# Optimization experiments

Measured on AMD Instinct MI355X. Metric: run time of the kernel, lower is better.

Reference implementation:

```python
import jax, jax.numpy as jnp
import numpy as np

D = 48


def setup_inputs() -> dict:
    key = jax.random.key(0)
    k1, k2, k3, k4, k5 = jax.random.split(key, 5)
    B, N, d = 4, 512, D
    x = jax.random.normal(k1, (B, N, d), dtype=jnp.float32)
    # Linear(2d, 2d) and Linear(2d, d); stored as (in, out) so y = x @ W + b
    s1 = 1.0 / np.sqrt(2 * d)
    W1 = jax.random.uniform(k2, (2 * d, 2 * d), dtype=jnp.float32, minval=-s1, maxval=s1)
    b1 = jax.random.uniform(k3, (2 * d,), dtype=jnp.float32, minval=-s1, maxval=s1)
    W2 = jax.random.uniform(k4, (2 * d, d), dtype=jnp.float32, minval=-s1, maxval=s1)
    b2 = jax.random.uniform(k5, (d,), dtype=jnp.float32, minval=-s1, maxval=s1)
    return {"x": x, "W1": W1, "b1": b1, "W2": W2, "b2": b2}


def reference(x, W1, b1, W2, b2):
    B, N, d = x.shape
    # pairwise concat: [B, N, N, 2d] with (i, j) = (x_i, x_j)
    xi = jnp.broadcast_to(x[:, :, None, :], (B, N, N, d))
    xj = jnp.broadcast_to(x[:, None, :, :], (B, N, N, d))
    cat = jnp.concatenate([xi, xj], axis=-1)
    h = jax.nn.gelu(cat @ W1 + b1, approximate=False)  # torch GELU is exact erf form
    p = h @ W2 + b2  # [B, N, N, d]
    mask = jnp.triu(jnp.ones((N, N), dtype=bool), 1)  # j > i masked
    p = jnp.where(mask[None, :, :, None], 0.0, p)
    w = jnp.sqrt(jnp.sum(p * p, axis=-1))  # frobenius norm over feature dim -> [B, N, N]
    w = jnp.where(mask[None, :, :], -1e9, w)
    w = jax.nn.softmax(w, axis=-1)[..., None]  # softmax over j
    return jnp.sum(w * p, axis=2)  # [B, N, d]
```

## Files before the change

### kernel.cpp

```cpp
#include <hip/hip_runtime.h>
#include <hip/hip_bf16.h>
#include <math.h>

#define DD 48
#define NN 512
#define TWO_D 96
#define ROWS 2048

typedef __attribute__((ext_vector_type(8))) short bf16x8;
typedef __attribute__((ext_vector_type(4))) float f32x4;
typedef __attribute__((ext_vector_type(2))) float f32x2;
typedef __attribute__((ext_vector_type(4))) unsigned int u32x4;

__device__ __forceinline__ f32x2 gelu_poly2(f32x2 u) {
    f32x2 lim;  lim  = 3.5777f;
    f32x2 nlim; nlim = -3.5777f;
    const f32x2 uc = __builtin_elementwise_min(__builtin_elementwise_max(u, nlim), lim);
    const f32x2 v = uc * uc;
    f32x2 c5; c5 = -1.04448e-6f;
    f32x2 c4; c4 = 4.61896e-5f;
    f32x2 c3; c3 = -8.62284e-4f;
    f32x2 c2; c2 = 9.22138e-3f;
    f32x2 c1; c1 = -6.58353e-2f;
    f32x2 c0; c0 = 3.98855e-1f;
    f32x2 E = __builtin_elementwise_fma(v, c5, c4);
    E = __builtin_elementwise_fma(v, E, c3);
    E = __builtin_elementwise_fma(v, E, c2);
    E = __builtin_elementwise_fma(v, E, c1);
    E = __builtin_elementwise_fma(v, E, c0);
    f32x2 hlf; hlf = 0.5f;
    return u * __builtin_elementwise_fma(uc, E, hlf);
}

__device__ __forceinline__ f32x2 bfpair(unsigned int w) {
    f32x2 r;
    r.x = __uint_as_float(w << 16);
    r.y = __uint_as_float(w & 0xffff0000u);
    return r;
}

__global__ __launch_bounds__(256) void precompute_kernel(
        const float* __restrict__ x,
        const float* __restrict__ W1,
        const float* __restrict__ b1,
        const float* __restrict__ W2,
        float* __restrict__ Aout,
        __hip_bfloat16* __restrict__ Bout,
        __hip_bfloat16* __restrict__ W2T) {
    if (blockIdx.x == ROWS / 4) {
        for (int idx = threadIdx.x; idx < DD * TWO_D; idx += 256) {
            const int f = idx / TWO_D;
            const int k = idx - f * TWO_D;
            W2T[idx] = __float2bfloat16(W2[k * DD + f]);
        }
        return;
    }
    const int wave = threadIdx.x >> 6;
    const int lane = threadIdx.x & 63;
    const int row = blockIdx.x * 4 + wave;
    __shared__ float xs[4][DD];
    if (threadIdx.x < 4 * DD)
        xs[threadIdx.x / DD][threadIdx.x % DD] = x[blockIdx.x * 4 * DD + threadIdx.x];
    __syncthreads();
    for (int t = lane; t < TWO_D; t += 64) {
        float a0 = 0.f, a1 = 0.f;
#pragma unroll 8
        for (int k = 0; k < DD; ++k) {
            const float xv = xs[wave][k];
            a0 = fmaf(xv, W1[k * TWO_D + t], a0);
            a1 = fmaf(xv, W1[(DD + k) * TWO_D + t], a1);
        }
        Aout[row * TWO_D + t] = a0 + b1[t];
        Bout[row * TWO_D + t] = __float2bfloat16(a1);
    }
}


#define LOAD_PB(PB_, PTR_)                                                      \
  { _Pragma("unroll")                                                           \
    for (int ks = 0; ks < 3; ++ks)                                              \
      PB_[ks] = *(const u32x4*)&(PTR_)[ks * 32 + q8]; }

#define CHUNK_MFMA(PB_, ACC_, PF_, NPTR_)                                       \
  { _Pragma("unroll")                                                           \
    for (int ks = 0; ks < 3; ++ks) {                                            \
      const unsigned int w0 = PB_[ks].x, w1 = PB_[ks].y,                        \
                         w2 = PB_[ks].z, w3 = PB_[ks].w;                        \
      if (PF_) PB_[ks] = *(const u32x4*)&(NPTR_)[ks * 32 + q8];                 \
      const f32x2 h0 = gelu_poly2(av2[ks][0] + bfpair(w0));                     \
      const f32x2 h1 = gelu_poly2(av2[ks][1] + bfpair(w1));                     \
      const f32x2 h2 = gelu_poly2(av2[ks][2] + bfpair(w2));                     \
      const f32x2 h3 = gelu_poly2(av2[ks][3] + bfpair(w3));                     \
      union { bf16x8 v; __hip_bfloat162 h2[4]; } hf;                            \
      hf.h2[0] = __float22bfloat162_rn(make_float2(h0.x, h0.y));                \
      hf.h2[1] = __float22bfloat162_rn(make_float2(h1.x, h1.y));                \
      hf.h2[2] = __float22bfloat162_rn(make_float2(h2.x, h2.y));                \
      hf.h2[3] = __float22bfloat162_rn(make_float2(h3.x, h3.y));                \
      ACC_[0] = __builtin_amdgcn_mfma_f32_16x16x32_bf16(bfrag[0][ks], hf.v, ACC_[0], 0, 0, 0); \
      ACC_[1] = __builtin_amdgcn_mfma_f32_16x16x32_bf16(bfrag[1][ks], hf.v, ACC_[1], 0, 0, 0); \
      ACC_[2] = __builtin_amdgcn_mfma_f32_16x16x32_bf16(bfrag[2][ks], hf.v, ACC_[2], 0, 0, 0); \
    } }

#define CHUNK_EPI(J0_, I_, ACC_, L_, O_)                                        \
  { f32x2 pv[3][2];                                                             \
    f32x2 ss2; ss2 = 0.f;                                                       \
    _Pragma("unroll")                                                           \
    for (int t = 0; t < 3; ++t) {                                               \
      f32x2 a01; a01.x = ACC_[t][0]; a01.y = ACC_[t][1];                        \
      f32x2 a23; a23.x = ACC_[t][2]; a23.y = ACC_[t][3];                        \
      pv[t][0] = a01 + b2v2[t][0];                                              \
      pv[t][1] = a23 + b2v2[t][1];                                              \
      ss2 = __builtin_elementwise_fma(pv[t][0], pv[t][0], ss2);                 \
      ss2 = __builtin_elementwise_fma(pv[t][1], pv[t][1], ss2);                 \
    }                                                                           \
    float ss = ss2.x + ss2.y;                                                   \
    ss += __shfl_xor(ss, 16);                                                   \
    ss += __shfl_xor(ss, 32);                                                   \
    const int j = (J0_) + n;                                                    \
    const float ew = (j <= (I_))                                                \
        ? __builtin_amdgcn_exp2f(sqrtf(ss) * 1.44269504f) : 0.f;                \
    L_ += ew;                                                                   \
    f32x2 ew2; ew2 = ew;                                                        \
    _Pragma("unroll")                                                           \
    for (int t = 0; t < 3; ++t) {                                               \
      O_[t][0] = __builtin_elementwise_fma(ew2, pv[t][0], O_[t][0]);            \
      O_[t][1] = __builtin_elementwise_fma(ew2, pv[t][1], O_[t][1]);            \
    } }

#define PROCESS_ROW_DUAL(I_, ROW_, CSTART_, L_, O_)                             \
  { f32x2 av2[3][4];                                                            \
    _Pragma("unroll")                                                           \
    for (int ks = 0; ks < 3; ++ks) {                                            \
      const float4 a0 = *(const float4*)&Arow[(size_t)(ROW_)*TWO_D + ks*32 + q8];     \
      const float4 a1 = *(const float4*)&Arow[(size_t)(ROW_)*TWO_D + ks*32 + q8 + 4]; \
      av2[ks][0].x=a0.x; av2[ks][0].y=a0.y; av2[ks][1].x=a0.z; av2[ks][1].y=a0.w;     \
      av2[ks][2].x=a1.x; av2[ks][2].y=a1.y; av2[ks][3].x=a1.z; av2[ks][3].y=a1.w;     \
    }                                                                           \
    const int nch = ((I_) + 16) >> 4;                                           \
    int c = (CSTART_);                                                          \
    const __hip_bfloat16* __restrict__ Bp =                                     \
        Bbase + (size_t)((c << 4) + n) * TWO_D;                                 \
    u32x4 pbA[3], pbB[3];                                                       \
    if (c < nch) LOAD_PB(pbA, Bp);                                              \
    if (c + 4 < nch) LOAD_PB(pbB, Bp + 64 * TWO_D);                             \
    for (; c + 4 < nch; c += 8) {                                               \
      const bool pfA = (c + 8) < nch;                                           \
      const bool pfB = (c + 12) < nch;                                          \
      const __hip_bfloat16* __restrict__ BpA = Bp + 128 * TWO_D;                \
      const __hip_bfloat16* __restrict__ BpB = Bp + 192 * TWO_D;                \
      f32x4 accA[3] = {{0.f,0.f,0.f,0.f},{0.f,0.f,0.f,0.f},{0.f,0.f,0.f,0.f}};  \
      f32x4 accB[3] = {{0.f,0.f,0.f,0.f},{0.f,0.f,0.f,0.f},{0.f,0.f,0.f,0.f}};  \
      CHUNK_MFMA(pbA, accA, pfA, BpA);                                          \
      CHUNK_MFMA(pbB, accB, pfB, BpB);                                          \
      CHUNK_EPI((c << 4), I_, accA, L_, O_);                                    \
      CHUNK_EPI(((c + 4) << 4), I_, accB, L_, O_);                              \
      Bp = BpA;                                                                 \
    }                                                                           \
    if (c < nch) {                                                              \
      f32x4 accA[3] = {{0.f,0.f,0.f,0.f},{0.f,0.f,0.f,0.f},{0.f,0.f,0.f,0.f}};  \
      CHUNK_MFMA(pbA, accA, false, Bp);                                         \
      CHUNK_EPI((c << 4), I_, accA, L_, O_);                                    \
    } }

__global__ __launch_bounds__(256) void pair_softmax_kernel(
        const float* __restrict__ Arow,
        const __hip_bfloat16* __restrict__ Brow,
        const __hip_bfloat16* __restrict__ W2T,
        const float* __restrict__ b2,
        float* __restrict__ out) {
    const int batch = blockIdx.x >> 8;
    const int pr = blockIdx.x & 255;
    const int iH = (NN - 1) - pr;
    const int iL = pr;
    const int cH = (iH >> 4) + 1;
    const int rowH = batch * NN + iH;
    const int rowL = batch * NN + iL;
    const __hip_bfloat16* __restrict__ Bbase = Brow + (size_t)batch * NN * TWO_D;

    const int tid = threadIdx.x;
    const int wave = tid >> 6;
    const int lane = tid & 63;
    const int n = lane & 15;
    const int q = lane >> 4;
    const int q8 = q * 8;

    bf16x8 bfrag[3][3];
#pragma unroll
    for (int t = 0; t < 3; ++t)
#pragma unroll
        for (int ks = 0; ks < 3; ++ks)
            bfrag[t][ks] = *(const bf16x8*)&W2T[(t * 16 + n) * TWO_D + ks * 32 + q8];
    f32x2 b2v2[3][2];
#pragma unroll
    for (int t = 0; t < 3; ++t) {
        b2v2[t][0].x = b2[t * 16 + 4 * q + 0];
        b2v2[t][0].y = b2[t * 16 + 4 * q + 1];
        b2v2[t][1].x = b2[t * 16 + 4 * q + 2];
        b2v2[t][1].y = b2[t * 16 + 4 * q + 3];
    }

    float lH = 0.f, lL = 0.f;
    f32x2 oH[3][2], oL[3][2];
#pragma unroll
    for (int t = 0; t < 3; ++t)
#pragma unroll
        for (int r = 0; r < 2; ++r) { oH[t][r] = 0.f; oL[t][r] = 0.f; }

    PROCESS_ROW_DUAL(iH, rowH, wave, lH, oH);
    const int cstartL = (wave + 128 - cH) & 3;
    PROCESS_ROW_DUAL(iL, rowL, cstartL, lL, oL);

#pragma unroll
    for (int d = 1; d <= 8; d <<= 1) {
        lH += __shfl_xor(lH, d);
        lL += __shfl_xor(lL, d);
#pragma unroll
        for (int t = 0; t < 3; ++t)
#pragma unroll
            for (int r = 0; r < 2; ++r) {
                oH[t][r].x += __shfl_xor(oH[t][r].x, d);
                oH[t][r].y += __shfl_xor(oH[t][r].y, d);
                oL[t][r].x += __shfl_xor(oL[t][r].x, d);
                oL[t][r].y += __shfl_xor(oL[t][r].y, d);
            }
    }
    __shared__ float lred[4][2];
    __shared__ float ored[4][2][DD];
    if (n == 0) {
#pragma unroll
        for (int t = 0; t < 3; ++t)
#pragma unroll
            for (int r = 0; r < 2; ++r) {
                ored[wave][0][t * 16 + 4 * q + 2 * r + 0] = oH[t][r].x;
                ored[wave][0][t * 16 + 4 * q + 2 * r + 1] = oH[t][r].y;
                ored[wave][1][t * 16 + 4 * q + 2 * r + 0] = oL[t][r].x;
                ored[wave][1][t * 16 + 4 * q + 2 * r + 1] = oL[t][r].y;
            }
    }
    if (lane == 0) { lred[wave][0] = lH; lred[wave][1] = lL; }
    __syncthreads();
    if (tid < 2 * DD) {
        const int sel = tid / DD;
        const int f = tid - sel * DD;
        float L = 0.f, O = 0.f;
#pragma unroll
        for (int wv = 0; wv < 4; ++wv) {
            L += lred[wv][sel];
            O += ored[wv][sel][f];
        }
        const int row = sel ? rowL : rowH;
        out[row * DD + f] = O / L;
    }
}

extern "C" void kernel_launch(void* const* d_in, const int* in_sizes, int n_in,
                              void* d_out, int out_size, void* d_ws, size_t ws_size,
                              hipStream_t stream) {
    const float* x  = (const float*)d_in[0];
    const float* W1 = (const float*)d_in[1];
    const float* b1 = (const float*)d_in[2];
    const float* W2 = (const float*)d_in[3];
    const float* b2 = (const float*)d_in[4];
    float* outp = (float*)d_out;

    float* A = (float*)d_ws;
    __hip_bfloat16* Bb  = (__hip_bfloat16*)(A + ROWS * TWO_D);
    __hip_bfloat16* W2T = Bb + ROWS * TWO_D;

    precompute_kernel<<<ROWS / 4 + 1, 256, 0, stream>>>(x, W1, b1, W2, A, Bb, W2T);
    pair_softmax_kernel<<<1024, 256, 0, stream>>>(A, Bb, W2T, b2, outp);
}
```

Before: 93.17 us.

## Switch pair kernel to fp16 with packed adds and LDS-staged W2 fragments

Moves the A/B projections and W2 from bf16/fp32 to fp16, so the A+B pre-activation is done with packed half2 adds and the MFMA uses the f16 variant. W2 fragments are staged in padded shared memory and reloaded per k-step instead of held in registers, and the two chunk streams are interleaved per k-step. The b2 bias is folded into the accumulator init, and the high-row results are reduced and flushed before the low row starts, which shortens register live ranges. The intent is to cut register pressure and VALU work in the hot loop. The cost is extra LDS reads and fp16 range/precision risk on the pre-activation sums.

```diff
diff --git a/kernel.cpp b/kernel.cpp
--- a/kernel.cpp
+++ b/kernel.cpp
@@ -1,16 +1,20 @@
 #include <hip/hip_runtime.h>
 #include <hip/hip_bf16.h>
+#include <hip/hip_fp16.h>
 #include <math.h>
 
 #define DD 48
 #define NN 512
 #define TWO_D 96
 #define ROWS 2048
-
-typedef __attribute__((ext_vector_type(8))) short bf16x8;
+#define W2P 104
+
+typedef __attribute__((ext_vector_type(8))) _Float16 f16x8;
 typedef __attribute__((ext_vector_type(4))) float f32x4;
 typedef __attribute__((ext_vector_type(2))) float f32x2;
 typedef __attribute__((ext_vector_type(4))) unsigned int u32x4;
+
+__device__ __forceinline__ __half2 h2cast(unsigned int u) { return __builtin_bit_cast(__half2, u); }
 
 __device__ __forceinline__ f32x2 gelu_poly2(f32x2 u) {
     f32x2 lim;  lim  = 3.5777f;
@@ -32,26 +36,19 @@
     return u * __builtin_elementwise_fma(uc, E, hlf);
 }
 
-__device__ __forceinline__ f32x2 bfpair(unsigned int w) {
-    f32x2 r;
-    r.x = __uint_as_float(w << 16);
-    r.y = __uint_as_float(w & 0xffff0000u);
-    return r;
-}
-
 __global__ __launch_bounds__(256) void precompute_kernel(
         const float* __restrict__ x,
         const float* __restrict__ W1,
         const float* __restrict__ b1,
         const float* __restrict__ W2,
-        float* __restrict__ Aout,
-        __hip_bfloat16* __restrict__ Bout,
-        __hip_bfloat16* __restrict__ W2T) {
+        __half* __restrict__ Aout,
+        __half* __restrict__ Bout,
+        __half* __restrict__ W2T) {
     if (blockIdx.x == ROWS / 4) {
         for (int idx = threadIdx.x; idx < DD * TWO_D; idx += 256) {
             const int f = idx / TWO_D;
             const int k = idx - f * TWO_D;
-            W2T[idx] = __float2bfloat16(W2[k * DD + f]);
+            W2T[idx] = __float2half(W2[k * DD + f]);
         }
         return;
     }
@@ -70,8 +67,8 @@
             a0 = fmaf(xv, W1[k * TWO_D + t], a0);
             a1 = fmaf(xv, W1[(DD + k) * TWO_D + t], a1);
         }
-        Aout[row * TWO_D + t] = a0 + b1[t];
-        Bout[row * TWO_D + t] = __float2bfloat16(a1);
+        Aout[row * TWO_D + t] = __float2half(a0 + b1[t]);
+        Bout[row * TWO_D + t] = __float2half(a1);
     }
 }
 
@@ -81,24 +78,41 @@
     for (int ks = 0; ks < 3; ++ks)                                              \
       PB_[ks] = *(const u32x4*)&(PTR_)[ks * 32 + q8]; }
 
-#define CHUNK_MFMA(PB_, ACC_, PF_, NPTR_)                                       \
+#define STREAM_KS(PB_, ACC_, PF_, NPTR_, KS_)                                   \
+  { const u32x4 aw = avp[KS_];                                                  \
+    const u32x4 bw = PB_[KS_];                                                  \
+    if (PF_) PB_[KS_] = *(const u32x4*)&(NPTR_)[(KS_) * 32 + q8];               \
+    const __half2 u0 = __hadd2(h2cast(aw.x), h2cast(bw.x));                     \
+    const __half2 u1 = __hadd2(h2cast(aw.y), h2cast(bw.y));                     \
+    const __half2 u2 = __hadd2(h2cast(aw.z), h2cast(bw.z));                     \
+    const __half2 u3 = __hadd2(h2cast(aw.w), h2cast(bw.w));                     \
+    f32x2 f0, f1, f2, f3;                                                       \
+    { float2 t_ = __half22float2(u0); f0.x = t_.x; f0.y = t_.y; }               \
+    { float2 t_ = __half22float2(u1); f1.x = t_.x; f1.y = t_.y; }               \
+    { float2 t_ = __half22float2(u2); f2.x = t_.x; f2.y = t_.y; }               \
+    { float2 t_ = __half22float2(u3); f3.x = t_.x; f3.y = t_.y; }               \
+    const f32x2 g0 = gelu_poly2(f0);                                            \
+    const f32x2 g1 = gelu_poly2(f1);                                            \
+    const f32x2 g2 = gelu_poly2(f2);                                            \
+    const f32x2 g3 = gelu_poly2(f3);                                            \
+    union { f16x8 v; __half2 h2[4]; } hf;                                       \
+    hf.h2[0] = __float22half2_rn(make_float2(g0.x, g0.y));                      \
+    hf.h2[1] = __float22half2_rn(make_float2(g1.x, g1.y));                      \
+    hf.h2[2] = __float22half2_rn(make_float2(g2.x, g2.y));                      \
+    hf.h2[3] = __float22half2_rn(make_float2(g3.x, g3.y));                      \
+    ACC_[0] = __builtin_amdgcn_mfma_f32_16x16x32_f16(bf0, hf.v, ACC_[0], 0, 0, 0); \
+    ACC_[1] = __builtin_amdgcn_mfma_f32_16x16x32_f16(bf1, hf.v, ACC_[1], 0, 0, 0); \
+    ACC_[2] = __builtin_amdgcn_mfma_f32_16x16x32_f16(bf2, hf.v, ACC_[2], 0, 0, 0); \
+  }
+
+#define FUSED_KS(PBa_, ACCa_, PFa_, NPa_, DOB_, PBb_, ACCb_, PFb_, NPb_)        \
   { _Pragma("unroll")                                                           \
-    for (int ks = 0; ks < 3; ++ks) {                                            \
-      const unsigned int w0 = PB_[ks].x, w1 = PB_[ks].y,                        \
-                         w2 = PB_[ks].z, w3 = PB_[ks].w;                        \
-      if (PF_) PB_[ks] = *(const u32x4*)&(NPTR_)[ks * 32 + q8];                 \
-      const f32x2 h0 = gelu_poly2(av2[ks][0] + bfpair(w0));                     \
-      const f32x2 h1 = gelu_poly2(av2[ks][1] + bfpair(w1));                     \
-      const f32x2 h2 = gelu_poly2(av2[ks][2] + bfpair(w2));                     \
-      const f32x2 h3 = gelu_poly2(av2[ks][3] + bfpair(w3));                     \
-      union { bf16x8 v; __hip_bfloat162 h2[4]; } hf;                            \
-      hf.h2[0] = __float22bfloat162_rn(make_float2(h0.x, h0.y));                \
-      hf.h2[1] = __float22bfloat162_rn(make_float2(h1.x, h1.y));                \
-      hf.h2[2] = __float22bfloat162_rn(make_float2(h2.x, h2.y));                \
-      hf.h2[3] = __float22bfloat162_rn(make_float2(h3.x, h3.y));                \
-      ACC_[0] = __builtin_amdgcn_mfma_f32_16x16x32_bf16(bfrag[0][ks], hf.v, ACC_[0], 0, 0, 0); \
-      ACC_[1] = __builtin_amdgcn_mfma_f32_16x16x32_bf16(bfrag[1][ks], hf.v, ACC_[1], 0, 0, 0); \
-      ACC_[2] = __builtin_amdgcn_mfma_f32_16x16x32_bf16(bfrag[2][ks], hf.v, ACC_[2], 0, 0, 0); \
+    for (int ksi = 0; ksi < 3; ++ksi) {                                         \
+      const f16x8 bf0 = *(const f16x8*)&w2s[(0 * 16 + n) * W2P + ksi * 32 + q8];\
+      const f16x8 bf1 = *(const f16x8*)&w2s[(1 * 16 + n) * W2P + ksi * 32 + q8];\
+      const f16x8 bf2 = *(const f16x8*)&w2s[(2 * 16 + n) * W2P + ksi * 32 + q8];\
+      STREAM_KS(PBa_, ACCa_, PFa_, NPa_, ksi);                                  \
+      if (DOB_) STREAM_KS(PBb_, ACCb_, PFb_, NPb_, ksi);                        \
     } }
 
 #define CHUNK_EPI(J0_, I_, ACC_, L_, O_)                                        \
@@ -106,10 +120,8 @@
     f32x2 ss2; ss2 = 0.f;                                                       \
     _Pragma("unroll")                                                           \
     for (int t = 0; t < 3; ++t) {                                               \
-      f32x2 a01; a01.x = ACC_[t][0]; a01.y = ACC_[t][1];                        \
-      f32x2 a23; a23.x = ACC_[t][2]; a23.y = ACC_[t][3];                        \
-      pv[t][0] = a01 + b2v2[t][0];                                              \
-      pv[t][1] = a23 + b2v2[t][1];                                              \
+      pv[t][0].x = ACC_[t][0]; pv[t][0].y = ACC_[t][1];                         \
+      pv[t][1].x = ACC_[t][2]; pv[t][1].y = ACC_[t][3];                         \
       ss2 = __builtin_elementwise_fma(pv[t][0], pv[t][0], ss2);                 \
       ss2 = __builtin_elementwise_fma(pv[t][1], pv[t][1], ss2);                 \
     }                                                                           \
@@ -127,45 +139,66 @@
       O_[t][1] = __builtin_elementwise_fma(ew2, pv[t][1], O_[t][1]);            \
     } }
 
+#define ACC_INIT(ACC_)                                                          \
+  { ACC_[0] = b2q[0]; ACC_[1] = b2q[1]; ACC_[2] = b2q[2]; }
+
 #define PROCESS_ROW_DUAL(I_, ROW_, CSTART_, L_, O_)                             \
-  { f32x2 av2[3][4];                                                            \
+  { u32x4 avp[3];                                                               \
     _Pragma("unroll")                                                           \
-    for (int ks = 0; ks < 3; ++ks) {                                            \
-      const float4 a0 = *(const float4*)&Arow[(size_t)(ROW_)*TWO_D + ks*32 + q8];     \
-      const float4 a1 = *(const float4*)&Arow[(size_t)(ROW_)*TWO_D + ks*32 + q8 + 4]; \
-      av2[ks][0].x=a0.x; av2[ks][0].y=a0.y; av2[ks][1].x=a0.z; av2[ks][1].y=a0.w;     \
-      av2[ks][2].x=a1.x; av2[ks][2].y=a1.y; av2[ks][3].x=a1.z; av2[ks][3].y=a1.w;     \
-    }                                                                           \
+    for (int ks = 0; ks < 3; ++ks)                                              \
+      avp[ks] = *(const u32x4*)&Arow[(size_t)(ROW_) * TWO_D + ks * 32 + q8];    \
     const int nch = ((I_) + 16) >> 4;                                           \
     int c = (CSTART_);                                                          \
-    const __hip_bfloat16* __restrict__ Bp =                                     \
-        Bbase + (size_t)((c << 4) + n) * TWO_D;                                 \
+    const __half* __restrict__ Bp = Bbase + (size_t)((c << 4) + n) * TWO_D;     \
     u32x4 pbA[3], pbB[3];                                                       \
     if (c < nch) LOAD_PB(pbA, Bp);                                              \
     if (c + 4 < nch) LOAD_PB(pbB, Bp + 64 * TWO_D);                             \
     for (; c + 4 < nch; c += 8) {                                               \
       const bool pfA = (c + 8) < nch;                                           \
       const bool pfB = (c + 12) < nch;                                          \
-      const __hip_bfloat16* __restrict__ BpA = Bp + 128 * TWO_D;                \
-      const __hip_bfloat16* __restrict__ BpB = Bp + 192 * TWO_D;                \
-      f32x4 accA[3] = {{0.f,0.f,0.f,0.f},{0.f,0.f,0.f,0.f},{0.f,0.f,0.f,0.f}};  \
-      f32x4 accB[3] = {{0.f,0.f,0.f,0.f},{0.f,0.f,0.f,0.f},{0.f,0.f,0.f,0.f}};  \
-      CHUNK_MFMA(pbA, accA, pfA, BpA);                                          \
-      CHUNK_MFMA(pbB, accB, pfB, BpB);                                          \
+      const __half* __restrict__ BpA = Bp + 128 * TWO_D;                        \
+      const __half* __restrict__ BpB = Bp + 192 * TWO_D;                        \
+      f32x4 accA[3], accB[3];                                                   \
+      ACC_INIT(accA); ACC_INIT(accB);                                           \
+      FUSED_KS(pbA, accA, pfA, BpA, true, pbB, accB, pfB, BpB);                 \
       CHUNK_EPI((c << 4), I_, accA, L_, O_);                                    \
       CHUNK_EPI(((c + 4) << 4), I_, accB, L_, O_);                              \
       Bp = BpA;                                                                 \
     }                                                                           \
     if (c < nch) {                                                              \
-      f32x4 accA[3] = {{0.f,0.f,0.f,0.f},{0.f,0.f,0.f,0.f},{0.f,0.f,0.f,0.f}};  \
-      CHUNK_MFMA(pbA, accA, false, Bp);                                         \
+      f32x4 accA[3];                                                            \
+      ACC_INIT(accA);                                                           \
+      FUSED_KS(pbA, accA, false, Bp, false, pbB, accA, false, Bp);              \
       CHUNK_EPI((c << 4), I_, accA, L_, O_);                                    \
     } }
 
+#define REDUCE_FLUSH(L_, O_, SEL_)                                              \
+  { _Pragma("unroll")                                                           \
+    for (int d = 1; d <= 8; d <<= 1) {                                          \
+      L_ += __shfl_xor(L_, d);                                                  \
+      _Pragma("unroll")                                                         \
+      for (int t = 0; t < 3; ++t)                                               \
+        _Pragma("unroll")                                                       \
+        for (int r = 0; r < 2; ++r) {                                           \
+          O_[t][r].x += __shfl_xor(O_[t][r].x, d);                              \
+          O_[t][r].y += __shfl_xor(O_[t][r].y, d);                              \
+        }                                                                       \
+    }                                                                           \
+    if (n == 0) {                                                               \
+      _Pragma("unroll")                                                         \
+      for (int t = 0; t < 3; ++t)                                               \
+        _Pragma("unroll")                                                       \
+        for (int r = 0; r < 2; ++r) {                                           \
+          ored[wave][SEL_][t * 16 + 4 * q + 2 * r + 0] = O_[t][r].x;            \
+          ored[wave][SEL_][t * 16 + 4 * q + 2 * r + 1] = O_[t][r].y;            \
+        }                                                                       \
+      if (q == 0) lred[wave][SEL_] = L_;                                        \
+    } }
+
 __global__ __launch_bounds__(256) void pair_softmax_kernel(
-        const float* __restrict__ Arow,
-        const __hip_bfloat16* __restrict__ Brow,
-        const __hip_bfloat16* __restrict__ W2T,
+        const __half* __restrict__ Arow,
+        const __half* __restrict__ Brow,
+        const __half* __restrict__ W2T,
         const float* __restrict__ b2,
         float* __restrict__ out) {
     const int batch = blockIdx.x >> 8;
@@ -175,7 +208,7 @@
     const int cH = (iH >> 4) + 1;
     const int rowH = batch * NN + iH;
     const int rowL = batch * NN + iL;
-    const __hip_bfloat16* __restrict__ Bbase = Brow + (size_t)batch * NN * TWO_D;
+    const __half* __restrict__ Bbase = Brow + (size_t)batch * NN * TWO_D;
 
     const int tid = threadIdx.x;
     const int wave = tid >> 6;
@@ -184,60 +217,43 @@
     const int q = lane >> 4;
     const int q8 = q * 8;
 
-    bf16x8 bfrag[3][3];
+    __shared__ __align__(16) __half w2s[DD * W2P];
+    __shared__ float lred[4][2];
+    __shared__ float ored[4][2][DD];
+
+    for (int idx = tid; idx < DD * TWO_D; idx += 256) {
+        const int f = idx / TWO_D;
+        const int k = idx - f * TWO_D;
+        w2s[f * W2P + k] = W2T[idx];
+    }
+    __syncthreads();
+
+    f32x4 b2q[3];
 #pragma unroll
     for (int t = 0; t < 3; ++t)
-#pragma unroll
-        for (int ks = 0; ks < 3; ++ks)
-            bfrag[t][ks] = *(const bf16x8*)&W2T[(t * 16 + n) * TWO_D + ks * 32 + q8];
-    f32x2 b2v2[3][2];
-#pragma unroll
-    for (int t = 0; t < 3; ++t) {
-        b2v2[t][0].x = b2[t * 16 + 4 * q + 0];
-        b2v2[t][0].y = b2[t * 16 + 4 * q + 1];
-        b2v2[t][1].x = b2[t * 16 + 4 * q + 2];
-        b2v2[t][1].y = b2[t * 16 + 4 * q + 3];
-    }
-
-    float lH = 0.f, lL = 0.f;
-    f32x2 oH[3][2], oL[3][2];
+        b2q[t] = *(const f32x4*)&b2[t * 16 + 4 * q];
+
+    float lH = 0.f;
+    f32x2 oH[3][2];
 #pragma unroll
     for (int t = 0; t < 3; ++t)
 #pragma unroll
-        for (int r = 0; r < 2; ++r) { oH[t][r] = 0.f; oL[t][r] = 0.f; }
+        for (int r = 0; r < 2; ++r) oH[t][r] = 0.f;
 
     PROCESS_ROW_DUAL(iH, rowH, wave, lH, oH);
+    REDUCE_FLUSH(lH, oH, 0);
+
+    float lL = 0.f;
+    f32x2 oL[3][2];
+#pragma unroll
+    for (int t = 0; t < 3; ++t)
+#pragma unroll
+        for (int r = 0; r < 2; ++r) oL[t][r] = 0.f;
+
     const int cstartL = (wave + 128 - cH) & 3;
     PROCESS_ROW_DUAL(iL, rowL, cstartL, lL, oL);
-
-#pragma unroll
-    for (int d = 1; d <= 8; d <<= 1) {
-        lH += __shfl_xor(lH, d);
-        lL += __shfl_xor(lL, d);
-#pragma unroll
-        for (int t = 0; t < 3; ++t)
-#pragma unroll
-            for (int r = 0; r < 2; ++r) {
-                oH[t][r].x += __shfl_xor(oH[t][r].x, d);
-                oH[t][r].y += __shfl_xor(oH[t][r].y, d);
-                oL[t][r].x += __shfl_xor(oL[t][r].x, d);
-                oL[t][r].y += __shfl_xor(oL[t][r].y, d);
-            }
-    }
-    __shared__ float lred[4][2];
-    __shared__ float ored[4][2][DD];
-    if (n == 0) {
-#pragma unroll
-        for (int t = 0; t < 3; ++t)
-#pragma unroll
-            for (int r = 0; r < 2; ++r) {
-                ored[wave][0][t * 16 + 4 * q + 2 * r + 0] = oH[t][r].x;
-                ored[wave][0][t * 16 + 4 * q + 2 * r + 1] = oH[t][r].y;
-                ored[wave][1][t * 16 + 4 * q + 2 * r + 0] = oL[t][r].x;
-                ored[wave][1][t * 16 + 4 * q + 2 * r + 1] = oL[t][r].y;
-            }
-    }
-    if (lane == 0) { lred[wave][0] = lH; lred[wave][1] = lL; }
+    REDUCE_FLUSH(lL, oL, 1);
+
     __syncthreads();
     if (tid < 2 * DD) {
         const int sel = tid / DD;
@@ -263,9 +279,9 @@
     const float* b2 = (const float*)d_in[4];
     float* outp = (float*)d_out;
 
-    float* A = (float*)d_ws;
-    __hip_bfloat16* Bb  = (__hip_bfloat16*)(A + ROWS * TWO_D);
-    __hip_bfloat16* W2T = Bb + ROWS * TWO_D;
+    __half* A   = (__half*)d_ws;
+    __half* Bb  = A + ROWS * TWO_D;
+    __half* W2T = Bb + ROWS * TWO_D;
 
     precompute_kernel<<<ROWS / 4 + 1, 256, 0, stream>>>(x, W1, b1, W2, A, Bb, W2T);
     pair_softmax_kernel<<<1024, 256, 0, stream>>>(A, Bb, W2T, b2, outp);
```

Result: no change. 92.75 us (-0.4%).
